# Optimization experiments

Hardware: AMD Instinct MI355X
Metric: run time of the kernel (lower is better)

## Reference

```python
import jax, jax.numpy as jnp
import numpy as np

B, N, D, E, R = 4, 4096, 64, 131072, 64

def setup_inputs() -> dict:
    key = jax.random.key(0)
    k1, k2, k3, k4 = jax.random.split(key, 4)
    z = jax.random.normal(k1, (B, N, D), dtype=jnp.float32)
    pairs = jax.random.randint(k2, (E, 2), 0, N, dtype=jnp.int64)
    # Linear params (PyTorch convention: y = x @ W.T + b), init scale ~ 1/sqrt(fan_in)
    W1 = jax.random.normal(k3, (R, 4 * D), dtype=jnp.float32) / np.sqrt(4 * D)
    b1 = jnp.zeros((R,), dtype=jnp.float32)
    W2 = jax.random.normal(k4, (R, R), dtype=jnp.float32) / np.sqrt(R)
    b2 = jnp.zeros((R,), dtype=jnp.float32)
    return {"z": z, "pairs": pairs, "W1": W1, "b1": b1, "W2": W2, "b2": b2}

def reference(z, pairs, W1, b1, W2, b2):
    # gather endpoint embeddings: [B, E, D]
    zi = z[:, pairs[:, 0], :]
    zj = z[:, pairs[:, 1], :]
    # pair feature [B, E, 4D]: concat(zi, zj, zi-zj, zi*zj)
    pair = jnp.concatenate([zi, zj, zi - zj, zi * zj], axis=-1)
    # 2-layer MLP (dropout is identity at inference)
    h = jnp.einsum('bef,rf->ber', pair, W1) + b1
    h = jax.nn.relu(h)
    h = jnp.einsum('ber,sr->bes', h, W2) + b2
    return h
```

## Files before the change

### kernel.cpp

```cpp
#include <hip/hip_runtime.h>
#include <hip/hip_bf16.h>
#include <stdint.h>


typedef __attribute__((ext_vector_type(8))) __bf16 bf16x8;
typedef __attribute__((ext_vector_type(4))) __bf16 bf16x4;
typedef __attribute__((ext_vector_type(4))) float  f32x4;

#define E_TOT 131072
#define N_TOK 4096
#define ROWS_PER_BLOCK 256
#define NSUB 4
#define Z_ELEMS (4 * N_TOK * 64)
#define WIMG_OFF (Z_ELEMS * 2)
#define WIMG_W_BYTES 32768
#define WIMG_B1 32768
#define WIMG_B2 33024

__device__ __forceinline__ bf16x8 pk8(float4 a, float4 b) {
    bf16x8 r;
    r[0] = (__bf16)a.x; r[1] = (__bf16)a.y; r[2] = (__bf16)a.z; r[3] = (__bf16)a.w;
    r[4] = (__bf16)b.x; r[5] = (__bf16)b.y; r[6] = (__bf16)b.z; r[7] = (__bf16)b.w;
    return r;
}
__device__ __forceinline__ float4 f4add(float4 a, float4 b){ return make_float4(a.x+b.x, a.y+b.y, a.z+b.z, a.w+b.w); }
__device__ __forceinline__ float4 f4sub(float4 a, float4 b){ return make_float4(a.x-b.x, a.y-b.y, a.z-b.z, a.w-b.w); }

__global__ __launch_bounds__(256) void prep_kernel(
    const float* __restrict__ z, const float* __restrict__ W1, const float* __restrict__ b1,
    const float* __restrict__ W2, const float* __restrict__ b2,
    __bf16* __restrict__ zw, char* __restrict__ wimg)
{
    const int tid = threadIdx.x;
    const int blk = blockIdx.x;
    if (blk < 512) {
        const int t = blk * 256 + tid;
        const float4 a = ((const float4*)z)[2 * t];
        const float4 b = ((const float4*)z)[2 * t + 1];
        ((bf16x8*)zw)[t] = pk8(a, b);
        return;
    }
    const int part = tid >> 6;
    const int scol = tid & 63;
    const int cswz = (scol & 7) << 4;
    if (part < 3) {
        const float* wr = W1 + (size_t)scol * 256;
        char* dst = wimg + scol * 384;
#pragma unroll
        for (int c8 = 0; c8 < 8; ++c8) {
            float4 p0, p1;
            if (part == 0) {
                float4 a0 = *(const float4*)(wr + c8*8);
                float4 a1 = *(const float4*)(wr + c8*8 + 4);
                float4 c0 = *(const float4*)(wr + 128 + c8*8);
                float4 c1 = *(const float4*)(wr + 128 + c8*8 + 4);
                p0 = f4add(a0, c0); p1 = f4add(a1, c1);
            } else if (part == 1) {
                float4 a0 = *(const float4*)(wr + 64 + c8*8);
                float4 a1 = *(const float4*)(wr + 64 + c8*8 + 4);
                float4 c0 = *(const float4*)(wr + 128 + c8*8);
                float4 c1 = *(const float4*)(wr + 128 + c8*8 + 4);
                p0 = f4sub(a0, c0); p1 = f4sub(a1, c1);
            } else {
                p0 = *(const float4*)(wr + 192 + c8*8);
                p1 = *(const float4*)(wr + 192 + c8*8 + 4);
            }
            *(bf16x8*)(dst + ((part * 128 + c8 * 16) ^ cswz)) = pk8(p0, p1);
        }
    } else {
        const float* wr = W2 + (size_t)scol * 64;
        char* dst = wimg + 24576 + scol * 128;
#pragma unroll
        for (int c8 = 0; c8 < 8; ++c8) {
            float4 p0 = *(const float4*)(wr + c8*8);
            float4 p1 = *(const float4*)(wr + c8*8 + 4);
            *(bf16x8*)(dst + ((c8 * 16) ^ cswz)) = pk8(p0, p1);
        }
    }
    if (tid < 64)            *(float*)(wimg + WIMG_B1 + 4 * tid) = b1[tid];
    else if (tid < 128)      *(float*)(wimg + WIMG_B2 + 4 * (tid - 64)) = b2[tid - 64];
}

__device__ __forceinline__ f32x4 mfma16(bf16x8 a, bf16x8 b, f32x4 c) {
    return __builtin_amdgcn_mfma_f32_16x16x32_bf16(a, b, c, 0, 0, 0);
}

__device__ __forceinline__ bf16x8 bmul(bf16x8 a, bf16x8 b) {
    bf16x8 r;
#pragma unroll
    for (int t = 0; t < 8; ++t)
        r[t] = (__bf16)((float)a[t] * (float)b[t]);
    return r;
}

__global__ __launch_bounds__(256, 4) void PairRelationEncoder_62775241998442_kernel(
    const __bf16* __restrict__ zw, const char* __restrict__ wimg,
    const int* __restrict__ pairs, float* __restrict__ out)
{
    const int tid  = threadIdx.x;
    const int wave = tid >> 6;
    const int lane = tid & 63;
    const int x = lane & 15;
    const int g = lane >> 4;

    const int bid = (int)(blockIdx.x & 7) * 256 + ((int)blockIdx.x >> 3);
    const int m0 = bid * ROWS_PER_BLOCK;
    const int b  = m0 >> 17;
    const int e0 = m0 & (E_TOT - 1);
    const __bf16* zb = zw + ((size_t)b * N_TOK * 64);

    int2 ijv[NSUB];
#pragma unroll
    for (int st = 0; st < NSUB; ++st)
        ijv[st] = *(const int2*)(pairs + 2 * (size_t)(e0 + (st * 4 + wave) * 16 + x));

    __shared__ char   wall[32768];
    __shared__ __bf16 h1s[4][1024];
    __shared__ float  b1s[64];
    __shared__ float  b2s[64];
    __bf16* h1w = h1s[wave];
    const char* w1b = wall;
    const char* w2b = wall + 24576;

#pragma unroll
    for (int r = 0; r < 8; ++r) {
        const int off = (r * 256 + tid) * 16;
        float4 v = *(const float4*)(wimg + off);
        *(float4*)(wall + off) = v;
    }
    if (tid < 64)            b1s[tid] = *(const float*)(wimg + WIMG_B1 + 4 * tid);
    else if (tid < 128)      b2s[tid - 64] = *(const float*)(wimg + WIMG_B2 + 4 * (tid - 64));

    __syncthreads();

    const int sw = (x & 7) << 4;

#pragma unroll
    for (int st = 0; st < NSUB; ++st) {
        const __bf16* zri = zb + (size_t)ijv[st].x * 64;
        const __bf16* zrj = zb + (size_t)ijv[st].y * 64;

        f32x4 acc[4];
#pragma unroll
        for (int ct = 0; ct < 4; ++ct)
            acc[ct] = *(const f32x4*)(b1s + ct * 16 + g * 4);

#pragma unroll
        for (int h = 0; h < 2; ++h) {
            bf16x8 azf = *(const bf16x8*)(zri + h * 32 + g * 8);
            bf16x8 bzf = *(const bf16x8*)(zrj + h * 32 + g * 8);
            bf16x8 pzf = bmul(azf, bzf);
            const int kb = h * 64 + g * 16;
#pragma unroll
            for (int ct = 0; ct < 4; ++ct) {
                const int colr = ct * 16 + x;
                const int cswz = (colr & 7) << 4;
                const char* wb = w1b + colr * 384;
                bf16x8 wzi = *(const bf16x8*)(wb + ((kb      ) ^ cswz));
                bf16x8 wzj = *(const bf16x8*)(wb + ((kb + 128) ^ cswz));
                bf16x8 wpr = *(const bf16x8*)(wb + ((kb + 256) ^ cswz));
                acc[ct] = mfma16(wzi, azf, acc[ct]);
                acc[ct] = mfma16(wzj, bzf, acc[ct]);
                acc[ct] = mfma16(wpr, pzf, acc[ct]);
            }
        }

#pragma unroll
        for (int ct = 0; ct < 4; ++ct) {
            bf16x4 p;
#pragma unroll
            for (int q = 0; q < 4; ++q)
                p[q] = (__bf16)fmaxf(acc[ct][q], 0.f);
            const int wo = (x * 128 + ct * 32 + g * 8) ^ sw;
            *(bf16x4*)((char*)h1w + wo) = p;
        }

        f32x4 o[4];
#pragma unroll
        for (int ct = 0; ct < 4; ++ct)
            o[ct] = *(const f32x4*)(b2s + ct * 16 + g * 4);

#pragma unroll
        for (int kk = 0; kk < 2; ++kk) {
            const int aoff = (x * 128 + kk * 64 + g * 16) ^ sw;
            const bf16x8 h1f = *(const bf16x8*)((const char*)h1w + aoff);
#pragma unroll
            for (int ct = 0; ct < 4; ++ct) {
                const int cols = ct * 16 + x;
                const bf16x8 w2f = *(const bf16x8*)(w2b + cols * 128
                                                    + ((kk * 64 + g * 16) ^ ((cols & 7) << 4)));
                o[ct] = mfma16(w2f, h1f, o[ct]);
            }
        }

        float* orow = out + ((size_t)(m0 + (st * 4 + wave) * 16 + x)) * 64;
#pragma unroll
        for (int ct = 0; ct < 4; ++ct)
            *(f32x4*)(orow + ct * 16 + g * 4) = o[ct];
    }
}

extern "C" void kernel_launch(void* const* d_in, const int* in_sizes, int n_in,
                              void* d_out, int out_size, void* d_ws, size_t ws_size,
                              hipStream_t stream) {
    const float* z     = (const float*)d_in[0];
    const int*   pairs = (const int*)  d_in[1];
    const float* W1    = (const float*)d_in[2];
    const float* b1    = (const float*)d_in[3];
    const float* W2    = (const float*)d_in[4];
    const float* b2    = (const float*)d_in[5];
    float* out = (float*)d_out;
    __bf16* zw  = (__bf16*)d_ws;
    char*   img = (char*)d_ws + WIMG_OFF;

    prep_kernel<<<513, 256, 0, stream>>>(z, W1, b1, W2, b2, zw, img);

    const int total_rows = 4 * E_TOT;
    dim3 grid(total_rows / ROWS_PER_BLOCK);
    PairRelationEncoder_62775241998442_kernel<<<grid, 256, 0, stream>>>(
        zw, img, pairs, out);
}
```

Baseline: 47.65 us.

## Process two sub-tiles per iteration to reuse weight fragments, keep biases in registers

The main loop now handles two 16-row sub-tiles together. Each W1/W2 fragment read from LDS feeds two MFMAs, which halves weight LDS traffic and leaves two independent accumulator chains to interleave. Biases now load straight from global into registers instead of through shared memory. The h1 scratch buffer doubles and the launch bound drops from 4 to 3 blocks per SM to make room for the extra registers, which may lower occupancy.

```diff
diff --git a/kernel.cpp b/kernel.cpp
--- a/kernel.cpp
+++ b/kernel.cpp
@@ -13,7 +13,6 @@
 #define NSUB 4
 #define Z_ELEMS (4 * N_TOK * 64)
 #define WIMG_OFF (Z_ELEMS * 2)
-#define WIMG_W_BYTES 32768
 #define WIMG_B1 32768
 #define WIMG_B2 33024
 
@@ -93,7 +92,7 @@
     return r;
 }
 
-__global__ __launch_bounds__(256, 4) void PairRelationEncoder_62775241998442_kernel(
+__global__ __launch_bounds__(256, 3) void PairRelationEncoder_62775241998442_kernel(
     const __bf16* __restrict__ zw, const char* __restrict__ wimg,
     const int* __restrict__ pairs, float* __restrict__ out)
 {
@@ -114,11 +113,17 @@
     for (int st = 0; st < NSUB; ++st)
         ijv[st] = *(const int2*)(pairs + 2 * (size_t)(e0 + (st * 4 + wave) * 16 + x));
 
+    f32x4 b1v[4], b2v[4];
+#pragma unroll
+    for (int ct = 0; ct < 4; ++ct) {
+        b1v[ct] = *(const f32x4*)(wimg + WIMG_B1 + (ct * 16 + g * 4) * 4);
+        b2v[ct] = *(const f32x4*)(wimg + WIMG_B2 + (ct * 16 + g * 4) * 4);
+    }
+
     __shared__ char   wall[32768];
-    __shared__ __bf16 h1s[4][1024];
-    __shared__ float  b1s[64];
-    __shared__ float  b2s[64];
-    __bf16* h1w = h1s[wave];
+    __shared__ __bf16 h1s[4][2048];
+    __bf16* h1A = h1s[wave];
+    __bf16* h1B = h1s[wave] + 1024;
     const char* w1b = wall;
     const char* w2b = wall + 24576;
 
@@ -128,75 +133,85 @@
         float4 v = *(const float4*)(wimg + off);
         *(float4*)(wall + off) = v;
     }
-    if (tid < 64)            b1s[tid] = *(const float*)(wimg + WIMG_B1 + 4 * tid);
-    else if (tid < 128)      b2s[tid - 64] = *(const float*)(wimg + WIMG_B2 + 4 * (tid - 64));
 
     __syncthreads();
 
     const int sw = (x & 7) << 4;
 
 #pragma unroll
-    for (int st = 0; st < NSUB; ++st) {
-        const __bf16* zri = zb + (size_t)ijv[st].x * 64;
-        const __bf16* zrj = zb + (size_t)ijv[st].y * 64;
-
-        f32x4 acc[4];
-#pragma unroll
-        for (int ct = 0; ct < 4; ++ct)
-            acc[ct] = *(const f32x4*)(b1s + ct * 16 + g * 4);
+    for (int sup = 0; sup < 2; ++sup) {
+        const int stA = 2 * sup, stB = 2 * sup + 1;
+        const __bf16* zriA = zb + (size_t)ijv[stA].x * 64;
+        const __bf16* zrjA = zb + (size_t)ijv[stA].y * 64;
+        const __bf16* zriB = zb + (size_t)ijv[stB].x * 64;
+        const __bf16* zrjB = zb + (size_t)ijv[stB].y * 64;
+
+        f32x4 accA[4], accB[4];
+#pragma unroll
+        for (int ct = 0; ct < 4; ++ct) { accA[ct] = b1v[ct]; accB[ct] = b1v[ct]; }
 
 #pragma unroll
         for (int h = 0; h < 2; ++h) {
-            bf16x8 azf = *(const bf16x8*)(zri + h * 32 + g * 8);
-            bf16x8 bzf = *(const bf16x8*)(zrj + h * 32 + g * 8);
-            bf16x8 pzf = bmul(azf, bzf);
+            bf16x8 azfA = *(const bf16x8*)(zriA + h * 32 + g * 8);
+            bf16x8 bzfA = *(const bf16x8*)(zrjA + h * 32 + g * 8);
+            bf16x8 pzfA = bmul(azfA, bzfA);
+            bf16x8 azfB = *(const bf16x8*)(zriB + h * 32 + g * 8);
+            bf16x8 bzfB = *(const bf16x8*)(zrjB + h * 32 + g * 8);
+            bf16x8 pzfB = bmul(azfB, bzfB);
             const int kb = h * 64 + g * 16;
 #pragma unroll
             for (int ct = 0; ct < 4; ++ct) {
-                const int colr = ct * 16 + x;
-                const int cswz = (colr & 7) << 4;
-                const char* wb = w1b + colr * 384;
-                bf16x8 wzi = *(const bf16x8*)(wb + ((kb      ) ^ cswz));
-                bf16x8 wzj = *(const bf16x8*)(wb + ((kb + 128) ^ cswz));
-                bf16x8 wpr = *(const bf16x8*)(wb + ((kb + 256) ^ cswz));
-                acc[ct] = mfma16(wzi, azf, acc[ct]);
-                acc[ct] = mfma16(wzj, bzf, acc[ct]);
-                acc[ct] = mfma16(wpr, pzf, acc[ct]);
+                const char* wb = w1b + (ct * 16 + x) * 384;
+                bf16x8 wzi = *(const bf16x8*)(wb + ((kb      ) ^ sw));
+                bf16x8 wzj = *(const bf16x8*)(wb + ((kb + 128) ^ sw));
+                bf16x8 wpr = *(const bf16x8*)(wb + ((kb + 256) ^ sw));
+                accA[ct] = mfma16(wzi, azfA, accA[ct]);
+                accB[ct] = mfma16(wzi, azfB, accB[ct]);
+                accA[ct] = mfma16(wzj, bzfA, accA[ct]);
+                accB[ct] = mfma16(wzj, bzfB, accB[ct]);
+                accA[ct] = mfma16(wpr, pzfA, accA[ct]);
+                accB[ct] = mfma16(wpr, pzfB, accB[ct]);
             }
         }
 
 #pragma unroll
         for (int ct = 0; ct < 4; ++ct) {
-            bf16x4 p;
-#pragma unroll
-            for (int q = 0; q < 4; ++q)
-                p[q] = (__bf16)fmaxf(acc[ct][q], 0.f);
+            bf16x4 pA, pB;
+#pragma unroll
+            for (int q = 0; q < 4; ++q) {
+                pA[q] = (__bf16)fmaxf(accA[ct][q], 0.f);
+                pB[q] = (__bf16)fmaxf(accB[ct][q], 0.f);
+            }
             const int wo = (x * 128 + ct * 32 + g * 8) ^ sw;
-            *(bf16x4*)((char*)h1w + wo) = p;
-        }
-
-        f32x4 o[4];
-#pragma unroll
-        for (int ct = 0; ct < 4; ++ct)
-            o[ct] = *(const f32x4*)(b2s + ct * 16 + g * 4);
+            *(bf16x4*)((char*)h1A + wo) = pA;
+            *(bf16x4*)((char*)h1B + wo) = pB;
+        }
+
+        f32x4 oA[4], oB[4];
+#pragma unroll
+        for (int ct = 0; ct < 4; ++ct) { oA[ct] = b2v[ct]; oB[ct] = b2v[ct]; }
 
 #pragma unroll
         for (int kk = 0; kk < 2; ++kk) {
             const int aoff = (x * 128 + kk * 64 + g * 16) ^ sw;
-            const bf16x8 h1f = *(const bf16x8*)((const char*)h1w + aoff);
+            const bf16x8 h1fA = *(const bf16x8*)((const char*)h1A + aoff);
+            const bf16x8 h1fB = *(const bf16x8*)((const char*)h1B + aoff);
 #pragma unroll
             for (int ct = 0; ct < 4; ++ct) {
-                const int cols = ct * 16 + x;
-                const bf16x8 w2f = *(const bf16x8*)(w2b + cols * 128
-                                                    + ((kk * 64 + g * 16) ^ ((cols & 7) << 4)));
-                o[ct] = mfma16(w2f, h1f, o[ct]);
-            }
-        }
-
-        float* orow = out + ((size_t)(m0 + (st * 4 + wave) * 16 + x)) * 64;
-#pragma unroll
-        for (int ct = 0; ct < 4; ++ct)
-            *(f32x4*)(orow + ct * 16 + g * 4) = o[ct];
+                const bf16x8 w2f = *(const bf16x8*)(w2b + (ct * 16 + x) * 128
+                                                    + ((kk * 64 + g * 16) ^ sw));
+                oA[ct] = mfma16(w2f, h1fA, oA[ct]);
+                oB[ct] = mfma16(w2f, h1fB, oB[ct]);
+            }
+        }
+
+        float* orowA = out + ((size_t)(m0 + (stA * 4 + wave) * 16 + x)) * 64;
+        float* orowB = out + ((size_t)(m0 + (stB * 4 + wave) * 16 + x)) * 64;
+#pragma unroll
+        for (int ct = 0; ct < 4; ++ct) {
+            *(f32x4*)(orowA + ct * 16 + g * 4) = oA[ct];
+            *(f32x4*)(orowB + ct * 16 + g * 4) = oB[ct];
+        }
     }
 }
 
```

Result: slower. 50.31 us (+5.6%).
